# Kernel tuning notes

Measured on AMD Instinct MI355X. Metric: run time of the kernel, lower is better.

The kernel has to match this reference:

```python
import jax, jax.numpy as jnp
import numpy as np

INP = 256
OUP = 256
FGROUP = 16
CGROUP = 8
K = 3
STRIDE = 1
PAD = K // 2
B, H, W = 16, 64, 64
O1 = OUP * INP * K * K // CGROUP  # 73728, glgf output channels


def setup_inputs() -> dict:
    key = jax.random.key(0)
    ks = jax.random.split(key, 11)
    s = 0.1  # keep sigmoid pre-activations in a sane range
    return {
        "x": jax.random.normal(ks[0], (B, INP, H, W), jnp.float32),
        # GLGF generating the dynamic conv weights (oup*inp*k*k//cgroup outputs)
        "g1_fc1_l": jax.random.normal(ks[1], (INP, INP // FGROUP), jnp.float32) * s,
        "g1_fc1_g1": jax.random.normal(ks[2], (FGROUP, INP // FGROUP), jnp.float32) * s,
        "g1_fc1_g2": jax.random.normal(ks[3], (INP, FGROUP), jnp.float32) * s,
        "g1_fc2_l": jax.random.normal(ks[4], (O1,), jnp.float32) * s,
        "g1_fc2_g": jax.random.normal(ks[5], (INP,), jnp.float32) * s,
        # GLGF generating the per-channel output gate c (oup outputs)
        "g2_fc1_l": jax.random.normal(ks[6], (INP, INP // FGROUP), jnp.float32) * s,
        "g2_fc1_g1": jax.random.normal(ks[7], (FGROUP, INP // FGROUP), jnp.float32) * s,
        "g2_fc1_g2": jax.random.normal(ks[8], (INP, FGROUP), jnp.float32) * s,
        "g2_fc2_l": jax.random.normal(ks[9], (OUP,), jnp.float32) * s,
        "g2_fc2_g": jax.random.normal(ks[10], (INP,), jnp.float32) * s,
    }


def glgf(g, w1l, w1g1, w1g2, w2l, w2g):
    """GLGF applied to a [B, inp] gap vector (all convs are 1x1 -> grouped linears)."""
    b, inp = g.shape
    gp = inp // FGROUP
    gg = g.reshape(b, FGROUP, gp)
    # wn_fc1_l: grouped (fgroup) inp->inp; weight [inp, inp//fgroup]
    local = jnp.einsum('bgi,goi->bgo', gg, w1l.reshape(FGROUP, gp, gp)).reshape(b, inp)
    # wn_fc1_g2(wn_fc1_g1(x)): inp->fgroup (grouped) then fgroup->inp (dense)
    glob = jnp.einsum('bgi,gi->bg', gg, w1g1) @ w1g2.T  # [b, inp]
    h = jax.nn.sigmoid(local + glob)
    # wn_fc2_l: groups=inp, inp->O; weight [O] (1 input channel per output)
    O = w2l.shape[0]
    local2 = (h[:, :, None] * w2l.reshape(inp, O // inp)).reshape(b, O)
    # wn_fc2_g: dense inp->1, broadcast-added
    glob2 = h @ w2g  # [b]
    return local2 + glob2[:, None]


def reference(x, g1_fc1_l, g1_fc1_g1, g1_fc1_g2, g1_fc2_l, g1_fc2_g,
              g2_fc1_l, g2_fc1_g1, g2_fc1_g2, g2_fc2_l, g2_fc2_g):
    b = x.shape[0]
    gap = x.mean(axis=(2, 3))  # adaptive_avg_pool2d to 1x1 -> [b, inp]
    # generate per-sample grouped conv weights: [b, oup, inp//cgroup, k, k]
    xw = glgf(gap, g1_fc1_l, g1_fc1_g1, g1_fc1_g2, g1_fc2_l, g1_fc2_g)
    w = xw.reshape(b, OUP, INP // CGROUP, K, K)
    # torch's groups=b*cgroup batch-trick == per-sample conv with groups=cgroup
    def conv_one(xi, wi):
        return jax.lax.conv_general_dilated(
            xi[None], wi, (STRIDE, STRIDE), [(PAD, PAD), (PAD, PAD)],
            feature_group_count=CGROUP,
            dimension_numbers=('NCHW', 'OIHW', 'NCHW'))[0]
    y = jax.vmap(conv_one)(x, w)  # [b, oup, H, W]
    # per-sample, per-channel gate
    c = glgf(gap, g2_fc1_l, g2_fc1_g1, g2_fc1_g2, g2_fc2_l, g2_fc2_g)  # [b, oup]
    return y * c[:, :, None, None]
```

## Files before the change

kernel.cpp:

```cpp
#include <hip/hip_runtime.h>
#include <cstddef>
#include <cstdint>

typedef __attribute__((ext_vector_type(8))) short bf16x8;
typedef __attribute__((ext_vector_type(8))) unsigned short ushort8v;
typedef __attribute__((ext_vector_type(16))) float f32x16;

__device__ __forceinline__ unsigned short f2bf(float f) {
  union { float f; unsigned u; } v; v.f = f;
  unsigned r = v.u + 0x7FFFu + ((v.u >> 16) & 1u);
  return (unsigned short)(r >> 16);
}

__global__ __launch_bounds__(256) void gap_kernel(const float* __restrict__ x,
                                                  float* __restrict__ gap) {
  const int bid = blockIdx.x;
  const float* p = x + (size_t)bid * 4096;
  const int t = threadIdx.x;
  float s = 0.f;
#pragma unroll
  for (int j = 0; j < 4; ++j) {
    const float4 v = *reinterpret_cast<const float4*>(p + j * 1024 + t * 4);
    s += v.x + v.y + v.z + v.w;
  }
#pragma unroll
  for (int off = 32; off > 0; off >>= 1) s += __shfl_down(s, off, 64);
  __shared__ float ws[4];
  if ((t & 63) == 0) ws[t >> 6] = s;
  __syncthreads();
  if (t == 0) gap[bid] = (ws[0] + ws[1] + ws[2] + ws[3]) * (1.f / 4096.f);
}

__global__ __launch_bounds__(256) void glgf_pack(
    const float* __restrict__ gap,
    const float* __restrict__ w1l, const float* __restrict__ w1g1,
    const float* __restrict__ w1g2, const float* __restrict__ w2l,
    const float* __restrict__ w2g,
    const float* __restrict__ v1l, const float* __restrict__ v1g1,
    const float* __restrict__ v1g2, const float* __restrict__ v2l,
    const float* __restrict__ v2g,
    unsigned short* __restrict__ wpack) {
  __shared__ float gapL[256];
  __shared__ float t1L[16];
  __shared__ float h1L[256];
  __shared__ float red[256];
  __shared__ float cLs[32];
  const int bid = blockIdx.x;
  const int bg = ((bid & 7) << 4) | (bid >> 3);
  const int g = bg & 7, b = bg >> 3;
  const int c = threadIdx.x;
  gapL[c] = gap[b * 256 + c];
  __syncthreads();

  const int gbase = c & ~15;
  float local1 = 0.f;
#pragma unroll
  for (int i = 0; i < 16; ++i) local1 += gapL[gbase + i] * w1l[c * 16 + i];
  if (c < 16) {
    float t = 0.f;
#pragma unroll
    for (int i = 0; i < 16; ++i) t += gapL[c * 16 + i] * w1g1[c * 16 + i];
    t1L[c] = t;
  }
  __syncthreads();
  float glob1 = 0.f;
#pragma unroll
  for (int gg = 0; gg < 16; ++gg) glob1 += t1L[gg] * w1g2[c * 16 + gg];
  const float h1 = 1.f / (1.f + expf(-(local1 + glob1)));
  h1L[c] = h1;
  red[c] = h1 * w2g[c];
  __syncthreads();
  for (int s = 128; s > 0; s >>= 1) {
    if (c < s) red[c] += red[c + s];
    __syncthreads();
  }
  const float glob2 = red[0];

  float local2 = 0.f;
#pragma unroll
  for (int i = 0; i < 16; ++i) local2 += gapL[gbase + i] * v1l[c * 16 + i];
  if (c < 16) {
    float t = 0.f;
#pragma unroll
    for (int i = 0; i < 16; ++i) t += gapL[c * 16 + i] * v1g1[c * 16 + i];
    t1L[c] = t;
  }
  __syncthreads();
  float glob1b = 0.f;
#pragma unroll
  for (int gg = 0; gg < 16; ++gg) glob1b += t1L[gg] * v1g2[c * 16 + gg];
  const float h2 = 1.f / (1.f + expf(-(local2 + glob1b)));
  red[c] = h2 * v2g[c];
  __syncthreads();
  for (int s = 128; s > 0; s >>= 1) {
    if (c < s) red[c] += red[c + s];
    __syncthreads();
  }
  if (c < 32) {
    const int o = g * 32 + c;
    float l = 0.f;
#pragma unroll
    for (int i = 0; i < 16; ++i) l += gapL[(o & ~15) + i] * v1l[o * 16 + i];
    float gl = 0.f;
#pragma unroll
    for (int gg = 0; gg < 16; ++gg) gl += t1L[gg] * v1g2[o * 16 + gg];
    const float h2o = 1.f / (1.f + expf(-(l + gl)));
    cLs[c] = h2o * v2l[o] + red[0];
  }
  __syncthreads();

  unsigned short* wpo = wpack + (size_t)bg * 9216;
#pragma unroll 4
  for (int it = 0; it < 36; ++it) {
    const int idx = it * 256 + c;
    const int kk = idx >> 9;
    const int rem = idx & 511;
    const int l = rem >> 3, e = rem & 7;
    const int oc = l & 31, hi = l >> 5;
    const int ic = ((kk & 1) << 4) + hi * 8 + e;
    const int sp = kk >> 1;
    const int o = (g << 5) + oc;
    const float wv = h1L[o] * w2l[o * 288 + ic * 9 + sp] + glob2;
    wpo[idx] = f2bf(wv * cLs[oc]);
  }
}

__global__ __launch_bounds__(512, 4) void conv_kernel(
    const float* __restrict__ x, const unsigned short* __restrict__ wpack,
    float* __restrict__ out) {
  __shared__ __align__(16) unsigned short wpl[9216];
  __shared__ __align__(16) unsigned short btile[21120];

  const int bid = blockIdx.x;
  const int wkr = ((bid & 7) << 7) | (bid >> 3);
  const int yq = wkr & 7;
  const int bg = wkr >> 3;
  const int g = bg & 7, b = bg >> 3;
  const int tid = threadIdx.x;
  const int lane = tid & 63, wave = tid >> 6;
  const int n = lane & 31, hi = lane >> 5;
  const int y0 = yq * 8;

  {
    const uint4* src = reinterpret_cast<const uint4*>(wpack + (size_t)bg * 9216);
    uint4* dst = reinterpret_cast<uint4*>(wpl);
#pragma unroll
    for (int i = 0; i < 3; ++i) {
      const int li = i * 512 + tid;
      if (li < 1152) dst[li] = src[li];
    }
  }

  const float* xg = x + (size_t)(b * 256 + g * 32) * 4096;
#pragma unroll
  for (int i = 0; i < 5; ++i) {
    const int t = wave * 5 + i;
    const int r = t >> 2, icq = t & 3;
    const int y = y0 - 1 + r;
    const bool ok = (y >= 0) && (y < 64);
    ushort8v cell;
#pragma unroll
    for (int j = 0; j < 8; ++j) {
      const float v = ok ? xg[(size_t)(icq * 8 + j) * 4096 + y * 64 + lane] : 0.f;
      cell[j] = f2bf(v);
    }
    const int px = lane + 1;
    *reinterpret_cast<ushort8v*>(
        &btile[((r * 4 + (icq ^ (px & 3))) * 66 + px) * 8]) = cell;
  }
  if (tid < 80) {
    const int r = tid >> 3, c8 = tid & 7;
    const int cq = c8 & 3, px = (c8 >> 2) ? 65 : 0;
    const ushort8v z = {0, 0, 0, 0, 0, 0, 0, 0};
    *reinterpret_cast<ushort8v*>(&btile[((r * 4 + cq) * 66 + px) * 8]) = z;
  }
  __syncthreads();

  f32x16 acc0, acc1;
#pragma unroll
  for (int i = 0; i < 16; ++i) { acc0[i] = 0.f; acc1[i] = 0.f; }

  __builtin_amdgcn_s_setprio(1);
#pragma unroll
  for (int kk = 0; kk < 18; ++kk) {
    const int sp = kk >> 1;
    const int ky = sp / 3, kx = sp % 3;
    const int cq = ((kk & 1) << 1) + hi;
    const int pxA = n + kx;
    const int pxB = 32 + n + kx;
    const bf16x8 af =
        *reinterpret_cast<const bf16x8*>(&wpl[kk * 512 + lane * 8]);
    const bf16x8 bf0 = *reinterpret_cast<const bf16x8*>(
        &btile[((((wave + ky) << 2) + (cq ^ (pxA & 3))) * 66 + pxA) * 8]);
    const bf16x8 bf1 = *reinterpret_cast<const bf16x8*>(
        &btile[((((wave + ky) << 2) + (cq ^ (pxB & 3))) * 66 + pxB) * 8]);
    acc0 = __builtin_amdgcn_mfma_f32_32x32x16_bf16(af, bf0, acc0, 0, 0, 0);
    acc1 = __builtin_amdgcn_mfma_f32_32x32x16_bf16(af, bf1, acc1, 0, 0, 0);
  }
  __builtin_amdgcn_s_setprio(0);

  const int y = y0 + wave;
  float* ob = out + (size_t)(b * 256 + g * 32) * 4096 + y * 64 + n +
              (size_t)(hi << 2) * 4096;
#pragma unroll
  for (int r = 0; r < 16; ++r) {
    const int row = (r & 3) + ((r >> 2) << 3);
    ob[(size_t)row * 4096] = acc0[r];
    ob[(size_t)row * 4096 + 32] = acc1[r];
  }
}

extern "C" void kernel_launch(void* const* d_in, const int* in_sizes, int n_in,
                              void* d_out, int out_size, void* d_ws,
                              size_t ws_size, hipStream_t stream) {
  const float* x    = (const float*)d_in[0];
  const float* w1l  = (const float*)d_in[1];
  const float* w1g1 = (const float*)d_in[2];
  const float* w1g2 = (const float*)d_in[3];
  const float* w2l  = (const float*)d_in[4];
  const float* w2g  = (const float*)d_in[5];
  const float* v1l  = (const float*)d_in[6];
  const float* v1g1 = (const float*)d_in[7];
  const float* v1g2 = (const float*)d_in[8];
  const float* v2l  = (const float*)d_in[9];
  const float* v2g  = (const float*)d_in[10];
  float* out = (float*)d_out;

  float* gap = (float*)d_ws;
  unsigned short* wpack = (unsigned short*)(gap + 4096);

  gap_kernel<<<4096, 256, 0, stream>>>(x, gap);
  glgf_pack<<<128, 256, 0, stream>>>(gap, w1l, w1g1, w1g2, w2l, w2g,
                                     v1l, v1g1, v1g2, v2l, v2g, wpack);
  conv_kernel<<<1024, 512, 0, stream>>>(x, wpack, out);
}
```

Before: 50.39 us.

## Restructure conv into 4-wave blocks with rolling row buffer and register prefetch

The conv kernel moves from 8 waves per block to 4 waves. Each block now processes its 8 output rows in four passes of two rows, keeping a 4-row input tile in LDS instead of 10 rows. The next input row is loaded into registers while the current pass runs its MFMAs, then written into LDS, so global loads overlap with compute and LDS use shrinks, which can allow more blocks per CU. The cost is extra barriers per pass, less MFMA work per wave between syncs, and accumulators held across all four passes before the stores.

```diff
diff --git a/kernel.cpp b/kernel.cpp
--- a/kernel.cpp
+++ b/kernel.cpp
@@ -125,11 +125,11 @@
   }
 }
 
-__global__ __launch_bounds__(512, 4) void conv_kernel(
+__global__ __launch_bounds__(256, 4) void conv_kernel(
     const float* __restrict__ x, const unsigned short* __restrict__ wpack,
     float* __restrict__ out) {
   __shared__ __align__(16) unsigned short wpl[9216];
-  __shared__ __align__(16) unsigned short btile[21120];
+  __shared__ __align__(16) unsigned short btile[8448];
 
   const int bid = blockIdx.x;
   const int wkr = ((bid & 7) << 7) | (bid >> 3);
@@ -139,36 +139,43 @@
   const int tid = threadIdx.x;
   const int lane = tid & 63, wave = tid >> 6;
   const int n = lane & 31, hi = lane >> 5;
+  const int wr = wave >> 1, wc = wave & 1;
   const int y0 = yq * 8;
+
+  const float* xg = x + (size_t)(b * 256 + g * 32) * 4096;
+  const int pxl = lane + 1;
+  const int swz = pxl & 3;
 
   {
     const uint4* src = reinterpret_cast<const uint4*>(wpack + (size_t)bg * 9216);
     uint4* dst = reinterpret_cast<uint4*>(wpl);
 #pragma unroll
-    for (int i = 0; i < 3; ++i) {
-      const int li = i * 512 + tid;
+    for (int i = 0; i < 5; ++i) {
+      const int li = i * 256 + tid;
       if (li < 1152) dst[li] = src[li];
     }
   }
 
-  const float* xg = x + (size_t)(b * 256 + g * 32) * 4096;
-#pragma unroll
-  for (int i = 0; i < 5; ++i) {
-    const int t = wave * 5 + i;
-    const int r = t >> 2, icq = t & 3;
-    const int y = y0 - 1 + r;
-    const bool ok = (y >= 0) && (y < 64);
-    ushort8v cell;
-#pragma unroll
-    for (int j = 0; j < 8; ++j) {
-      const float v = ok ? xg[(size_t)(icq * 8 + j) * 4096 + y * 64 + lane] : 0.f;
-      cell[j] = f2bf(v);
-    }
-    const int px = lane + 1;
+  ushort8v st[4];
+  {
+    const int y = y0 - 1 + wave;
+    const bool ok = (y >= 0);
+#pragma unroll
+    for (int icq = 0; icq < 4; ++icq) {
+      ushort8v cell;
+#pragma unroll
+      for (int j = 0; j < 8; ++j) {
+        const float v = ok ? xg[(size_t)(icq * 8 + j) * 4096 + y * 64 + lane] : 0.f;
+        cell[j] = f2bf(v);
+      }
+      st[icq] = cell;
+    }
+  }
+#pragma unroll
+  for (int icq = 0; icq < 4; ++icq)
     *reinterpret_cast<ushort8v*>(
-        &btile[((r * 4 + (icq ^ (px & 3))) * 66 + px) * 8]) = cell;
-  }
-  if (tid < 80) {
+        &btile[((wave * 4 + (icq ^ swz)) * 66 + pxl) * 8]) = st[icq];
+  if (tid < 32) {
     const int r = tid >> 3, c8 = tid & 7;
     const int cq = c8 & 3, px = (c8 >> 2) ? 65 : 0;
     const ushort8v z = {0, 0, 0, 0, 0, 0, 0, 0};
@@ -176,37 +183,64 @@
   }
   __syncthreads();
 
-  f32x16 acc0, acc1;
-#pragma unroll
-  for (int i = 0; i < 16; ++i) { acc0[i] = 0.f; acc1[i] = 0.f; }
-
-  __builtin_amdgcn_s_setprio(1);
-#pragma unroll
-  for (int kk = 0; kk < 18; ++kk) {
-    const int sp = kk >> 1;
-    const int ky = sp / 3, kx = sp % 3;
-    const int cq = ((kk & 1) << 1) + hi;
-    const int pxA = n + kx;
-    const int pxB = 32 + n + kx;
-    const bf16x8 af =
-        *reinterpret_cast<const bf16x8*>(&wpl[kk * 512 + lane * 8]);
-    const bf16x8 bf0 = *reinterpret_cast<const bf16x8*>(
-        &btile[((((wave + ky) << 2) + (cq ^ (pxA & 3))) * 66 + pxA) * 8]);
-    const bf16x8 bf1 = *reinterpret_cast<const bf16x8*>(
-        &btile[((((wave + ky) << 2) + (cq ^ (pxB & 3))) * 66 + pxB) * 8]);
-    acc0 = __builtin_amdgcn_mfma_f32_32x32x16_bf16(af, bf0, acc0, 0, 0, 0);
-    acc1 = __builtin_amdgcn_mfma_f32_32x32x16_bf16(af, bf1, acc1, 0, 0, 0);
-  }
-  __builtin_amdgcn_s_setprio(0);
-
-  const int y = y0 + wave;
-  float* ob = out + (size_t)(b * 256 + g * 32) * 4096 + y * 64 + n +
-              (size_t)(hi << 2) * 4096;
-#pragma unroll
-  for (int r = 0; r < 16; ++r) {
-    const int row = (r & 3) + ((r >> 2) << 3);
-    ob[(size_t)row * 4096] = acc0[r];
-    ob[(size_t)row * 4096 + 32] = acc1[r];
+  f32x16 acc[4];
+#pragma unroll
+  for (int p = 0; p < 4; ++p) {
+    if (p > 0) {
+#pragma unroll
+      for (int icq = 0; icq < 4; ++icq)
+        *reinterpret_cast<ushort8v*>(
+            &btile[((wave * 4 + (icq ^ swz)) * 66 + pxl) * 8]) = st[icq];
+      __syncthreads();
+    }
+
+    if (p < 3) {
+      const int y = y0 + (p + 1) * 2 - 1 + wave;
+      const bool ok = (y < 64);
+#pragma unroll
+      for (int icq = 0; icq < 4; ++icq) {
+        ushort8v cell;
+#pragma unroll
+        for (int j = 0; j < 8; ++j) {
+          const float v = ok ? xg[(size_t)(icq * 8 + j) * 4096 + y * 64 + lane] : 0.f;
+          cell[j] = f2bf(v);
+        }
+        st[icq] = cell;
+      }
+    }
+
+#pragma unroll
+    for (int i = 0; i < 16; ++i) acc[p][i] = 0.f;
+
+    __builtin_amdgcn_s_setprio(1);
+#pragma unroll
+    for (int kk = 0; kk < 18; ++kk) {
+      const int sp = kk >> 1;
+      const int ky = sp / 3, kx = sp % 3;
+      const int px2 = wc * 32 + n + kx;
+      const int cq = ((kk & 1) << 1) + hi;
+      const bf16x8 af =
+          *reinterpret_cast<const bf16x8*>(&wpl[kk * 512 + lane * 8]);
+      const bf16x8 bf = *reinterpret_cast<const bf16x8*>(
+          &btile[((((wr + ky) << 2) + (cq ^ (px2 & 3))) * 66 + px2) * 8]);
+      acc[p] = __builtin_amdgcn_mfma_f32_32x32x16_bf16(af, bf, acc[p], 0, 0, 0);
+    }
+    __builtin_amdgcn_s_setprio(0);
+
+    if (p < 3) __syncthreads();
+  }
+
+  float* ob0 = out + (size_t)(b * 256 + g * 32) * 4096 + wc * 32 + n +
+               (size_t)(hi << 2) * 4096;
+#pragma unroll
+  for (int p = 0; p < 4; ++p) {
+    const int y = y0 + p * 2 + wr;
+    float* ob = ob0 + y * 64;
+#pragma unroll
+    for (int r = 0; r < 16; ++r) {
+      const int row = (r & 3) + ((r >> 2) << 3);
+      ob[(size_t)row * 4096] = acc[p][r];
+    }
   }
 }
 
@@ -232,5 +266,5 @@
   gap_kernel<<<4096, 256, 0, stream>>>(x, gap);
   glgf_pack<<<128, 256, 0, stream>>>(gap, w1l, w1g1, w1g2, w2l, w2g,
                                      v1l, v1g1, v1g2, v2l, v2g, wpack);
-  conv_kernel<<<1024, 512, 0, stream>>>(x, wpack, out);
-}
+  conv_kernel<<<1024, 256, 0, stream>>>(x, wpack, out);
+}
```

Measured after the change: 53.17 us. 5.5% more time.
